# Kernel tuning notes

Hardware: AMD Instinct MI355X
Metric: run time of the kernel (lower is better)

Reference implementation:

```python
import jax, jax.numpy as jnp
import numpy as np

HIDDEN = 1024
HEADS = 16
HEAD_DIM = HIDDEN // HEADS
B, S = 2, 2048


def setup_inputs() -> dict:
    key = jax.random.key(0)
    ks = jax.random.split(key, 7)
    scale = 1.0 / np.sqrt(HIDDEN)
    return {
        "hidden_states": jax.random.normal(ks[0], (B, S, HIDDEN), dtype=jnp.float32),
        "Wq": jax.random.normal(ks[1], (HIDDEN, HIDDEN), dtype=jnp.float32) * scale,
        "bq": jax.random.normal(ks[2], (HIDDEN,), dtype=jnp.float32) * 0.02,
        "Wk": jax.random.normal(ks[3], (HIDDEN, HIDDEN), dtype=jnp.float32) * scale,
        "bk": jax.random.normal(ks[4], (HIDDEN,), dtype=jnp.float32) * 0.02,
        "Wv": jax.random.normal(ks[5], (HIDDEN, HIDDEN), dtype=jnp.float32) * scale,
        "bv": jax.random.normal(ks[6], (HIDDEN,), dtype=jnp.float32) * 0.02,
    }


def reference(hidden_states, Wq, bq, Wk, bk, Wv, bv):
    # QKV projections: [B,S,H] -> [B,S,heads,head_dim]
    def proj(W, b):
        y = jnp.einsum('bsh,hd->bsd', hidden_states, W) + b
        return y.reshape(B, S, HEADS, HEAD_DIM)

    q = proj(Wq, bq)
    k = proj(Wk, bk)
    v = proj(Wv, bv)

    # scores: [B,heads,Sq,Sk]
    scores = jnp.einsum('bqnd,bknd->bnqk', q, k) / jnp.sqrt(
        jnp.asarray(HEAD_DIM, dtype=hidden_states.dtype))
    probs = jax.nn.softmax(scores, axis=-1)  # dropout is identity at inference
    ctx = jnp.einsum('bnqk,bknd->bqnd', probs, v)
    return ctx.reshape(B, S, HIDDEN)
```

## Files before the change

### kernel.cpp

```cpp
#include <hip/hip_runtime.h>

#define HID 1024
#define SEQ 2048
#define NB  2
#define NH  16
#define HD  64
#define M_ROWS (NB*SEQ)

typedef _Float16 half8 __attribute__((ext_vector_type(8)));
typedef _Float16 half4 __attribute__((ext_vector_type(4)));
typedef float    f32x4 __attribute__((ext_vector_type(4)));
typedef unsigned uint4v __attribute__((ext_vector_type(4)));

#define GLOAD_LDS16(g, l) \
  __builtin_amdgcn_global_load_lds((const __attribute__((address_space(1))) void*)(g), \
                                   (__attribute__((address_space(3))) void*)(l), 16, 0, 0)

#define QSCL 0.18033688011112042f

#define CVT_PK_U32(a, b) __builtin_bit_cast(unsigned, __builtin_amdgcn_cvt_pkrtz((a), (b)))

__device__ __forceinline__ float exp2_raw(float x) {
  float r;
  asm("v_exp_f32 %0, %1" : "=v"(r) : "v"(x));
  return r;
}


__global__ __launch_bounds__(256) void cvt_x(const float* __restrict__ in,
                                             _Float16* __restrict__ out, int n4) {
  int i = blockIdx.x * 256 + threadIdx.x;
  int stride = gridDim.x * 256;
  for (; i < n4; i += stride) {
    float4 v = ((const float4*)in)[i];
    half4 o;
    o[0] = (_Float16)v.x; o[1] = (_Float16)v.y;
    o[2] = (_Float16)v.z; o[3] = (_Float16)v.w;
    ((half4*)out)[i] = o;
  }
}

__global__ __launch_bounds__(256) void cvt_w(const float* __restrict__ W0,
                                             const float* __restrict__ W1,
                                             const float* __restrict__ W2,
                                             _Float16* __restrict__ Wt) {
  __shared__ __align__(16) _Float16 tl[64 * 72];
  const int z = blockIdx.z;
  const float* W = (z == 0) ? W0 : (z == 1) ? W1 : W2;
  const int k0 = blockIdx.x * 64, n0 = blockIdx.y * 64;
  const int tid = threadIdx.x;
  const int kk = tid >> 4;
  const int nn = (tid & 15) * 4;
#pragma unroll
  for (int r = 0; r < 4; ++r) {
    int k = kk + r * 16;
    float4 v = *(const float4*)&W[(size_t)(k0 + k) * HID + n0 + nn];
    tl[(nn + 0) * 72 + k] = (_Float16)v.x;
    tl[(nn + 1) * 72 + k] = (_Float16)v.y;
    tl[(nn + 2) * 72 + k] = (_Float16)v.z;
    tl[(nn + 3) * 72 + k] = (_Float16)v.w;
  }
  __syncthreads();
#pragma unroll
  for (int r = 0; r < 2; ++r) {
    int c = r * 256 + tid;
    int n = c >> 3, kc = (c & 7) * 8;
    half8 o = *(const half8*)&tl[n * 72 + kc];
    *(half8*)&Wt[(size_t)z * HID * HID + (size_t)(n0 + n) * HID + k0 + kc] = o;
  }
}

__global__ __launch_bounds__(256) void qkv_gemm(const _Float16* __restrict__ X,
                                                const _Float16* __restrict__ Wt,
                                                const float* __restrict__ bq,
                                                const float* __restrict__ bk,
                                                const float* __restrict__ bv,
                                                _Float16* __restrict__ QKV) {
  __shared__ __align__(16) _Float16 Al[128 * 64];
  __shared__ __align__(16) _Float16 Bl[128 * 64];
  const int tid = threadIdx.x;
  const int lane = tid & 63;
  const int wid = tid >> 6;
  const int wr = wid >> 1, wc = wid & 1;
  const int g = lane >> 4, qi = lane & 15;
  const int r0 = blockIdx.x * 128;
  const int c0 = blockIdx.y * 128;
  const int z = blockIdx.z;
  const _Float16* Wz = Wt + (size_t)z * HID * HID;
  const float* bias = (z == 0) ? bq : (z == 1) ? bk : bv;
  const float scl = (z == 0) ? QSCL : 1.0f;
  _Float16* Out = QKV + (size_t)z * M_ROWS * HID;

  f32x4 acc[4][4];
#pragma unroll
  for (int m = 0; m < 4; ++m)
#pragma unroll
    for (int n = 0; n < 4; ++n) acc[m][n] = (f32x4){0.f, 0.f, 0.f, 0.f};

  for (int kt = 0; kt < 16; ++kt) {
    const int kb = kt * 64;
#pragma unroll
    for (int it = 0; it < 4; ++it) {
      int c = it * 256 + tid;
      int row = c >> 3, ci = c & 7;
      int sc = (ci ^ (row & 7)) * 8;
      GLOAD_LDS16(X + (size_t)(r0 + row) * HID + kb + sc, &Al[c * 8]);
      GLOAD_LDS16(Wz + (size_t)(c0 + row) * HID + kb + sc, &Bl[c * 8]);
    }
    __syncthreads();
#pragma unroll
    for (int ks = 0; ks < 2; ++ks) {
      half8 a[4], b[4];
#pragma unroll
      for (int m = 0; m < 4; ++m) {
        int row = wr * 64 + m * 16 + qi;
        int off = row * 64 + (((ks * 4 + g) ^ (row & 7)) * 8);
        a[m] = *(const half8*)&Al[off];
      }
#pragma unroll
      for (int n = 0; n < 4; ++n) {
        int col = wc * 64 + n * 16 + qi;
        int off = col * 64 + (((ks * 4 + g) ^ (col & 7)) * 8);
        b[n] = *(const half8*)&Bl[off];
      }
#pragma unroll
      for (int m = 0; m < 4; ++m)
#pragma unroll
        for (int n = 0; n < 4; ++n)
          acc[m][n] = __builtin_amdgcn_mfma_f32_16x16x32_f16(a[m], b[n], acc[m][n], 0, 0, 0);
    }
    __syncthreads();
  }
#pragma unroll
  for (int n = 0; n < 4; ++n) {
    int col = c0 + wc * 64 + n * 16 + qi;
    float bv_ = bias[col];
#pragma unroll
    for (int m = 0; m < 4; ++m) {
      int row = r0 + wr * 64 + m * 16 + g * 4;
#pragma unroll
      for (int r = 0; r < 4; ++r)
        Out[(size_t)(row + r) * HID + col] = (_Float16)((acc[m][n][r] + bv_) * scl);
    }
  }
}

__global__ __launch_bounds__(256) void vt_transpose(const _Float16* __restrict__ V,
                                                    _Float16* __restrict__ Vt) {
  __shared__ __align__(16) _Float16 tl[64 * 64];
  const int tid = threadIdx.x;
  const int bh = blockIdx.y, b = bh >> 4, h = bh & 15;
  const int s0 = blockIdx.x * 64;
#pragma unroll
  for (int it = 0; it < 2; ++it) {
    int c = it * 256 + tid;
    int s = c >> 3, d8 = c & 7;
    half8 v = *(const half8*)&V[(size_t)(b * SEQ + s0 + s) * HID + h * 64 + d8 * 8];
    *(half8*)&tl[s * 64 + (d8 ^ (s & 7)) * 8] = v;
  }
  __syncthreads();
#pragma unroll
  for (int it = 0; it < 2; ++it) {
    int d = (tid >> 3) + it * 32;
    int sg = tid & 7;
    half8 o;
#pragma unroll
    for (int e = 0; e < 8; ++e) {
      int s = 32 * (sg >> 2) + 4 * (sg & 3) + (e & 3) + 16 * (e >> 2);
      o[e] = tl[s * 64 + ((d >> 3) ^ (s & 7)) * 8 + (d & 7)];
    }
    *(half8*)&Vt[(size_t)bh * HD * SEQ + (size_t)d * SEQ + s0 + sg * 8] = o;
  }
}

__global__ __launch_bounds__(512, 4) void attn(const _Float16* __restrict__ Q,
                                               const _Float16* __restrict__ K,
                                               const _Float16* __restrict__ Vt,
                                               float* __restrict__ Out) {
  __shared__ __align__(16) _Float16 Kl[4][64 * 64];
  __shared__ __align__(16) _Float16 Vl[4][64 * 64];

  const int tid = threadIdx.x;
  const int lane = tid & 63;
  const int w = tid >> 6;
  const int g = lane >> 4, qi = lane & 15;
  const int nl = (blockIdx.x & 7) * 32 + (blockIdx.x >> 3);
  const int qb = nl & 7;
  const int bh = nl >> 3;
  const int b = bh >> 4, h = bh & 15;
  const size_t baseq = (size_t)b * SEQ * HID + (size_t)h * HD;
  const size_t basev = (size_t)bh * HD * SEQ;
  const int q0 = qb * 256 + w * 32;

  half8 qf[2][2];
#pragma unroll
  for (int cfr = 0; cfr < 2; ++cfr)
#pragma unroll
    for (int ks = 0; ks < 2; ++ks)
      qf[cfr][ks] = *(const half8*)&Q[baseq + (size_t)(q0 + cfr * 16 + qi) * HID + ks * 32 + g * 8];

  half8 ones;
#pragma unroll
  for (int j = 0; j < 8; ++j) ones[j] = (qi == 0) ? (_Float16)1.0f : (_Float16)0.0f;

  int offA[2][4];
#pragma unroll
  for (int ks = 0; ks < 2; ++ks)
#pragma unroll
    for (int fr = 0; fr < 4; ++fr) {
      int row = fr * 16 + qi;
      offA[ks][fr] = row * 64 + (((ks * 4 + g) ^ (row & 7)) * 8);
    }

  f32x4 ctx[4][2];
#pragma unroll
  for (int fr = 0; fr < 4; ++fr)
#pragma unroll
    for (int cfr = 0; cfr < 2; ++cfr) ctx[fr][cfr] = (f32x4){0.f, 0.f, 0.f, 0.f};
  f32x4 c5[2] = {(f32x4){0.f, 0.f, 0.f, 0.f}, (f32x4){0.f, 0.f, 0.f, 0.f}};

#define STAGE(buf, tt) do {                                                        \
    const int kv_ = (tt) * 64;                                                     \
    int row_ = tid >> 3, ci_ = tid & 7;                                            \
    int sc_ = (ci_ ^ (row_ & 7)) * 8;                                              \
    GLOAD_LDS16(K + baseq + (size_t)(kv_ + row_) * HID + sc_, &Kl[buf][tid * 8]);  \
    GLOAD_LDS16(Vt + basev + (size_t)row_ * SEQ + kv_ + sc_, &Vl[buf][tid * 8]);   \
  } while (0)

  STAGE(0, 0);
  STAGE(1, 1);

  for (int t = 0; t < 32; ++t) {
    const int cur = t & 3;
    const int nt = (t + 2 < 32) ? t + 2 : 31;
    STAGE((t + 2) & 3, nt);
    asm volatile("s_waitcnt vmcnt(4)" ::: "memory");
    __builtin_amdgcn_s_barrier();
    asm volatile("" ::: "memory");

    f32x4 sf[4][2];
#pragma unroll
    for (int fr = 0; fr < 4; ++fr)
#pragma unroll
      for (int cfr = 0; cfr < 2; ++cfr) sf[fr][cfr] = (f32x4){0.f, 0.f, 0.f, 0.f};
    __builtin_amdgcn_s_setprio(1);
#pragma unroll
    for (int ks = 0; ks < 2; ++ks) {
      half8 ak[4];
#pragma unroll
      for (int fr = 0; fr < 4; ++fr) ak[fr] = *(const half8*)&Kl[cur][offA[ks][fr]];
#pragma unroll
      for (int fr = 0; fr < 4; ++fr)
#pragma unroll
        for (int cfr = 0; cfr < 2; ++cfr)
          sf[fr][cfr] = __builtin_amdgcn_mfma_f32_16x16x32_f16(ak[fr], qf[cfr][ks], sf[fr][cfr], 0, 0, 0);
    }
    __builtin_amdgcn_s_setprio(0);

    unsigned wp[2][8];
#pragma unroll
    for (int cfr = 0; cfr < 2; ++cfr)
#pragma unroll
      for (int fr = 0; fr < 4; ++fr) {
        wp[cfr][2 * fr]     = CVT_PK_U32(exp2_raw(sf[fr][cfr][0]), exp2_raw(sf[fr][cfr][1]));
        wp[cfr][2 * fr + 1] = CVT_PK_U32(exp2_raw(sf[fr][cfr][2]), exp2_raw(sf[fr][cfr][3]));
      }

    __builtin_amdgcn_s_setprio(1);
#pragma unroll
    for (int ks = 0; ks < 2; ++ks) {
      half8 av[4];
#pragma unroll
      for (int fr = 0; fr < 4; ++fr) av[fr] = *(const half8*)&Vl[cur][offA[ks][fr]];
      half8 pb[2];
#pragma unroll
      for (int cfr = 0; cfr < 2; ++cfr) {
        uint4v uu = {wp[cfr][4 * ks], wp[cfr][4 * ks + 1], wp[cfr][4 * ks + 2], wp[cfr][4 * ks + 3]};
        pb[cfr] = __builtin_bit_cast(half8, uu);
      }
#pragma unroll
      for (int fr = 0; fr < 4; ++fr)
#pragma unroll
        for (int cfr = 0; cfr < 2; ++cfr)
          ctx[fr][cfr] = __builtin_amdgcn_mfma_f32_16x16x32_f16(av[fr], pb[cfr], ctx[fr][cfr], 0, 0, 0);
#pragma unroll
      for (int cfr = 0; cfr < 2; ++cfr)
        c5[cfr] = __builtin_amdgcn_mfma_f32_16x16x32_f16(ones, pb[cfr], c5[cfr], 0, 0, 0);
    }
    __builtin_amdgcn_s_setprio(0);
  }
#undef STAGE
  asm volatile("s_waitcnt vmcnt(0)" ::: "memory");

#pragma unroll
  for (int cfr = 0; cfr < 2; ++cfr) {
    float tot = __shfl(c5[cfr][0], qi, 64);
    float inv = 1.f / tot;
    int qrow = q0 + cfr * 16 + qi;
#pragma unroll
    for (int fr = 0; fr < 4; ++fr) {
      float4 o;
      o.x = ctx[fr][cfr][0] * inv;
      o.y = ctx[fr][cfr][1] * inv;
      o.z = ctx[fr][cfr][2] * inv;
      o.w = ctx[fr][cfr][3] * inv;
      *(float4*)&Out[baseq + (size_t)qrow * HID + fr * 16 + g * 4] = o;
    }
  }
}


extern "C" void kernel_launch(void* const* d_in, const int* in_sizes, int n_in,
                              void* d_out, int out_size, void* d_ws, size_t ws_size,
                              hipStream_t stream) {
  (void)in_sizes; (void)n_in; (void)out_size; (void)ws_size;
  const float* hs = (const float*)d_in[0];
  const float* Wq = (const float*)d_in[1];
  const float* bq = (const float*)d_in[2];
  const float* Wk = (const float*)d_in[3];
  const float* bk = (const float*)d_in[4];
  const float* Wv = (const float*)d_in[5];
  const float* bv = (const float*)d_in[6];
  float* out = (float*)d_out;

  _Float16* Xh  = (_Float16*)d_ws;
  _Float16* Wt  = Xh + (size_t)M_ROWS * HID;
  _Float16* QKV = Wt + (size_t)3 * HID * HID;
  _Float16* Vt  = Xh;

  cvt_x<<<1024, 256, 0, stream>>>(hs, Xh, (M_ROWS * HID) / 4);
  cvt_w<<<dim3(16, 16, 3), 256, 0, stream>>>(Wq, Wk, Wv, Wt);
  qkv_gemm<<<dim3(32, 8, 3), 256, 0, stream>>>(Xh, Wt, bq, bk, bv, QKV);
  vt_transpose<<<dim3(32, 32), 256, 0, stream>>>(QKV + (size_t)2 * M_ROWS * HID, Vt);
  attn<<<256, 512, 0, stream>>>(QKV,
                                QKV + (size_t)M_ROWS * HID,
                                Vt,
                                out);
}
```

Before: 99.78 us.

## Double-buffer LDS tiles in QKV GEMM to overlap global loads with MFMA

The QKV projection GEMM now keeps two LDS buffers for the A and B tiles. It issues the global-to-LDS loads for the next k-tile right after the barrier, so they overlap with the MFMA work on the current tile, and the trailing per-iteration barrier is dropped. This doubles LDS use to 64KB per block, which may cut occupancy. Correctness relies on the single barrier at the top of each iteration, placed after the vmcnt(0) wait, to order reads of the previous buffer against its overwrite.

```diff
diff --git a/kernel.cpp b/kernel.cpp
--- a/kernel.cpp
+++ b/kernel.cpp
@@ -76,8 +76,8 @@
                                                 const float* __restrict__ bk,
                                                 const float* __restrict__ bv,
                                                 _Float16* __restrict__ QKV) {
-  __shared__ __align__(16) _Float16 Al[128 * 64];
-  __shared__ __align__(16) _Float16 Bl[128 * 64];
+  __shared__ __align__(16) _Float16 Al[2][128 * 64];
+  __shared__ __align__(16) _Float16 Bl[2][128 * 64];
   const int tid = threadIdx.x;
   const int lane = tid & 63;
   const int wid = tid >> 6;
@@ -97,17 +97,27 @@
 #pragma unroll
     for (int n = 0; n < 4; ++n) acc[m][n] = (f32x4){0.f, 0.f, 0.f, 0.f};
 
+#define GSTAGE(buf, kt) do {                                                        \
+    const int kb_ = (kt) * 64;                                                      \
+    _Pragma("unroll")                                                               \
+    for (int it_ = 0; it_ < 4; ++it_) {                                             \
+      int c_ = it_ * 256 + tid;                                                     \
+      int row_ = c_ >> 3, ci_ = c_ & 7;                                             \
+      int sc_ = (ci_ ^ (row_ & 7)) * 8;                                             \
+      GLOAD_LDS16(X + (size_t)(r0 + row_) * HID + kb_ + sc_, &Al[buf][c_ * 8]);     \
+      GLOAD_LDS16(Wz + (size_t)(c0 + row_) * HID + kb_ + sc_, &Bl[buf][c_ * 8]);    \
+    }                                                                               \
+  } while (0)
+
+  GSTAGE(0, 0);
+
   for (int kt = 0; kt < 16; ++kt) {
-    const int kb = kt * 64;
-#pragma unroll
-    for (int it = 0; it < 4; ++it) {
-      int c = it * 256 + tid;
-      int row = c >> 3, ci = c & 7;
-      int sc = (ci ^ (row & 7)) * 8;
-      GLOAD_LDS16(X + (size_t)(r0 + row) * HID + kb + sc, &Al[c * 8]);
-      GLOAD_LDS16(Wz + (size_t)(c0 + row) * HID + kb + sc, &Bl[c * 8]);
-    }
-    __syncthreads();
+    const int cur = kt & 1;
+    asm volatile("s_waitcnt vmcnt(0)" ::: "memory");
+    __builtin_amdgcn_s_barrier();
+    asm volatile("" ::: "memory");
+    if (kt < 15) GSTAGE(cur ^ 1, kt + 1);
+
 #pragma unroll
     for (int ks = 0; ks < 2; ++ks) {
       half8 a[4], b[4];
@@ -115,13 +125,13 @@
       for (int m = 0; m < 4; ++m) {
         int row = wr * 64 + m * 16 + qi;
         int off = row * 64 + (((ks * 4 + g) ^ (row & 7)) * 8);
-        a[m] = *(const half8*)&Al[off];
+        a[m] = *(const half8*)&Al[cur][off];
       }
 #pragma unroll
       for (int n = 0; n < 4; ++n) {
         int col = wc * 64 + n * 16 + qi;
         int off = col * 64 + (((ks * 4 + g) ^ (col & 7)) * 8);
-        b[n] = *(const half8*)&Bl[off];
+        b[n] = *(const half8*)&Bl[cur][off];
       }
 #pragma unroll
       for (int m = 0; m < 4; ++m)
@@ -129,8 +139,9 @@
         for (int n = 0; n < 4; ++n)
           acc[m][n] = __builtin_amdgcn_mfma_f32_16x16x32_f16(a[m], b[n], acc[m][n], 0, 0, 0);
     }
-    __syncthreads();
-  }
+  }
+#undef GSTAGE
+
 #pragma unroll
   for (int n = 0; n < 4; ++n) {
     int col = c0 + wc * 64 + n * 16 + qi;
```

Measured after the change: 100.2 us. Within noise of the previous version (+0.4%).
